# Performance work log

Hardware: AMD Instinct MI355X
Metric: run time of the kernel (lower is better)

Reference implementation:

```python
import jax, jax.numpy as jnp
import numpy as np

B, S, D, H = 2, 2048, 1024, 16
DK = D // H  # 64


def setup_inputs() -> dict:
    key = jax.random.key(0)
    ks = jax.random.split(key, 8)
    q = jax.random.normal(ks[0], (B, S, D), dtype=jnp.float32)
    k = jax.random.normal(ks[1], (B, S, D), dtype=jnp.float32)
    v = jax.random.normal(ks[2], (B, S, D), dtype=jnp.float32)
    mask = jax.random.randint(ks[3], (B, 1, S, S), 0, 2, dtype=jnp.int32)
    scale = 1.0 / np.sqrt(D)
    Wq = jax.random.normal(ks[4], (D, D), dtype=jnp.float32) * scale
    Wk = jax.random.normal(ks[5], (D, D), dtype=jnp.float32) * scale
    Wv = jax.random.normal(ks[6], (D, D), dtype=jnp.float32) * scale
    Wo = jax.random.normal(ks[7], (D, D), dtype=jnp.float32) * scale
    return {"q": q, "k": k, "v": v, "mask": mask,
            "Wq": Wq, "Wk": Wk, "Wv": Wv, "Wo": Wo}


def reference(q, k, v, mask, Wq, Wk, Wv, Wo):
    # Linear projections (torch nn.Linear: x @ W.T, no bias)
    qh = (q @ Wq.T).reshape(B, S, H, DK).transpose(0, 2, 1, 3)  # [B,H,S,DK]
    kh = (k @ Wk.T).reshape(B, S, H, DK).transpose(0, 2, 1, 3)
    vh = (v @ Wv.T).reshape(B, S, H, DK).transpose(0, 2, 1, 3)
    # Scaled dot-product attention with mask fill of -1e9 where mask == 0
    scores = jnp.einsum('bhqd,bhkd->bhqk', qh, kh) / jnp.sqrt(jnp.float32(DK))
    scores = jnp.where(mask == 0, jnp.float32(-1e9), scores)
    attn = jax.nn.softmax(scores, axis=-1)
    ctx = jnp.einsum('bhqk,bhkd->bhqd', attn, vh)  # [B,H,S,DK]
    ctx = ctx.transpose(0, 2, 1, 3).reshape(B, S, D)
    return ctx @ Wo.T
```

## Files before the change

### kernel.cpp

```cpp
#include <hip/hip_runtime.h>

using u16    = unsigned short;
using u32    = unsigned int;
using f32x4  = __attribute__((ext_vector_type(4))) float;
using f32x16 = __attribute__((ext_vector_type(16))) float;
using bf16x8 = __attribute__((ext_vector_type(8))) __bf16;
using u16x4  = __attribute__((ext_vector_type(4))) u16;
using u16x8  = __attribute__((ext_vector_type(8))) u16;
using u32x2  = __attribute__((ext_vector_type(2))) u32;
using u32x4  = __attribute__((ext_vector_type(4))) u32;
using i32x4  = __attribute__((ext_vector_type(4))) int;


__device__ __forceinline__ u16 f2bf(float f) {
  union { __bf16 b; u16 u; } c; c.b = (__bf16)f; return c.u;
}

typedef __attribute__((address_space(1))) const void GVoid;
typedef __attribute__((address_space(3))) void LVoid;

__device__ __forceinline__ void gload_lds16(const void* g, void* l) {
  __builtin_amdgcn_global_load_lds((GVoid*)g, (LVoid*)l, 16, 0, 0);
}

__global__ void cvt_w(const float* __restrict__ a, const float* __restrict__ b,
                      const float* __restrict__ c, const float* __restrict__ dd,
                      u16* __restrict__ oa, u16* __restrict__ ob,
                      u16* __restrict__ oc, u16* __restrict__ od) {
  int y = blockIdx.y;
  const float* s = (y == 0) ? a : (y == 1) ? b : (y == 2) ? c : dd;
  u16* d = (y == 0) ? oa : (y == 1) ? ob : (y == 2) ? oc : od;
  int i = blockIdx.x * 256 + threadIdx.x;
  f32x4 v = ((const f32x4*)s)[i];
  u16x4 r;
#pragma unroll
  for (int j = 0; j < 4; ++j) r[j] = f2bf(v[j]);
  ((u16x4*)d)[i] = r;
}

__global__ void pack_mask(const int* __restrict__ m, u32* __restrict__ mp) {
  int tid = blockIdx.x * 256 + threadIdx.x;
  int q = tid & 2047, kt = (tid >> 11) & 31, b = tid >> 16;
  const i32x4* src = (const i32x4*)(m + ((size_t)(b * 2048 + q)) * 2048 + kt * 64);
  u32 w0 = 0, w1 = 0;
#pragma unroll
  for (int j = 0; j < 8; ++j) {
    i32x4 a = src[j], c = src[j + 8];
#pragma unroll
    for (int e = 0; e < 4; ++e) {
      w0 |= (a[e] != 0 ? 1u : 0u) << (j * 4 + e);
      w1 |= (c[e] != 0 ? 1u : 0u) << (j * 4 + e);
    }
  }
  ((u32x2*)mp)[((size_t)(b * 32 + kt)) * 2048 + q] = u32x2{w0, w1};
}

__global__ __launch_bounds__(256, 3) void gemm_qkv(const float* __restrict__ Aq,
                                                   const float* __restrict__ Ak,
                                                   const float* __restrict__ Av,
                                                   const u16* __restrict__ Wb,
                                                   u16* __restrict__ out) {
  __shared__ alignas(16) char lds[49152];
  const int t = threadIdx.x;
  const int lane = t & 63, wid = t >> 6;
  const int g = lane >> 4, r16 = lane & 15;
  const int wm = wid >> 1, wn = wid & 1;
  const int m0 = blockIdx.x * 128, n0 = blockIdx.y * 128;
  const int z = blockIdx.z;

  const float* Axf = (z == 0) ? Aq : (z == 1) ? Ak : Av;
  const char* Ab = (const char*)Axf;
  const char* Bb = (const char*)(Wb + (size_t)z * 1048576);
  u16* op = out + (size_t)z * 4194304;
  const float qsc = (z == 0) ? 0.18033688011f : 1.0f;

  f32x4 acc[4][4] = {};

  for (int kk = 0; kk < 1024; kk += 64) {
#pragma unroll
    for (int i = 0; i < 8; ++i) {
      int ci = i * 256 + t;
      int row = ci >> 4;
      int pc = ci & 15;
      int lc = pc ^ (row & 15);
      gload_lds16(Ab + (size_t)(m0 + row) * 4096 + kk * 4 + lc * 16, lds + ci * 16);
    }
#pragma unroll
    for (int i = 0; i < 4; ++i) {
      int ci = i * 256 + t;
      int row = ci >> 3;
      int cbs = ((ci & 7) << 4) ^ ((row & 7) << 4);
      gload_lds16(Bb + (size_t)(n0 + row) * 2048 + kk * 2 + cbs, lds + 32768 + ci * 16);
    }
    __syncthreads();
#pragma unroll
    for (int kc = 0; kc < 2; ++kc) {
      bf16x8 af[4], bfr[4];
#pragma unroll
      for (int mf = 0; mf < 4; ++mf) {
        int row = wm * 64 + mf * 16 + r16;
        const char* arow = lds + row * 256;
        int x = row & 15;
        int lc0 = 8 * kc + 2 * g;
        f32x4 alo = *(const f32x4*)(arow + ((lc0 ^ x) * 16));
        f32x4 ahi = *(const f32x4*)(arow + (((lc0 + 1) ^ x) * 16));
        u16x8 pk;
#pragma unroll
        for (int j = 0; j < 4; ++j) { pk[j] = f2bf(alo[j]); pk[4 + j] = f2bf(ahi[j]); }
        af[mf] = __builtin_bit_cast(bf16x8, pk);
      }
#pragma unroll
      for (int nf = 0; nf < 4; ++nf) {
        int row = wn * 64 + nf * 16 + r16;
        bfr[nf] = *(const bf16x8*)(lds + 32768 + row * 128 +
                                   ((64 * kc + 16 * g) ^ ((row & 7) << 4)));
      }
#pragma unroll
      for (int mf = 0; mf < 4; ++mf)
#pragma unroll
        for (int nf = 0; nf < 4; ++nf)
          acc[mf][nf] = __builtin_amdgcn_mfma_f32_16x16x32_bf16(af[mf], bfr[nf], acc[mf][nf], 0, 0, 0);
    }
    __syncthreads();
  }

#pragma unroll
  for (int mf = 0; mf < 4; ++mf) {
#pragma unroll
    for (int nf = 0; nf < 4; ++nf) {
      int mb = m0 + wm * 64 + mf * 16 + 4 * g;
      int n = n0 + wn * 64 + nf * 16 + r16;
      if (z == 0) {
        int bb = mb >> 11, h = n >> 6, dk = n & 63;
#pragma unroll
        for (int r = 0; r < 4; ++r) {
          int s2 = (mb + r) & 2047;
          op[((size_t)(bb * 16 + h) * 2048 + s2) * 64 + dk] = f2bf(acc[mf][nf][r] * qsc);
        }
      } else if (z == 1) {
        int h = n >> 6, dk = n & 63;
#pragma unroll
        for (int r = 0; r < 4; ++r) {
          int m = mb + r;
          int bb = m >> 11, s2 = m & 2047;
          size_t off16 = ((((size_t)(bb * 16 + h) * 32 + (s2 >> 6)) * 2 + ((s2 >> 5) & 1)) * 8 +
                          (dk >> 3)) * 32 + (s2 & 31);
          op[off16 * 8 + (dk & 7)] = f2bf(acc[mf][nf][r]);
        }
      } else {
        int bb = mb >> 11, s2 = mb & 2047, h = n >> 6, d = n & 63;
        size_t off16 = ((((size_t)(bb * 16 + h) * 32 + (s2 >> 6)) * 8 + ((s2 & 63) >> 3)) * 2 +
                        (d >> 5)) * 32 + (d & 31);
        u16x4 pv;
#pragma unroll
        for (int r = 0; r < 4; ++r) pv[r] = f2bf(acc[mf][nf][r]);
        *(u16x4*)(op + off16 * 8 + (s2 & 7)) = pv;
      }
    }
  }
}

__global__ __launch_bounds__(256, 2) void gemm_out(const u16* __restrict__ X,
                                                   const u16* __restrict__ W,
                                                   float* __restrict__ out) {
  __shared__ alignas(16) char lds[32768];
  const int t = threadIdx.x;
  const int lane = t & 63, wid = t >> 6;
  const int g = lane >> 4, r16 = lane & 15;
  const int wm = wid >> 1, wn = wid & 1;
  const int m0 = blockIdx.x * 128, n0 = blockIdx.y * 128;
  const char* Ab = (const char*)X;
  const char* Bb = (const char*)W;

  f32x4 acc[4][4] = {};

  for (int kk = 0; kk < 1024; kk += 64) {
#pragma unroll
    for (int i = 0; i < 4; ++i) {
      int ci = i * 256 + t;
      int row = ci >> 3;
      int cbs = ((ci & 7) << 4) ^ ((row & 7) << 4);
      gload_lds16(Ab + (size_t)(m0 + row) * 2048 + kk * 2 + cbs, lds + ci * 16);
      gload_lds16(Bb + (size_t)(n0 + row) * 2048 + kk * 2 + cbs, lds + 16384 + ci * 16);
    }
    __syncthreads();
#pragma unroll
    for (int kc = 0; kc < 2; ++kc) {
      bf16x8 af[4], bfr[4];
#pragma unroll
      for (int mf = 0; mf < 4; ++mf) {
        int row = wm * 64 + mf * 16 + r16;
        af[mf] = *(const bf16x8*)(lds + row * 128 + ((64 * kc + 16 * g) ^ ((row & 7) << 4)));
      }
#pragma unroll
      for (int nf = 0; nf < 4; ++nf) {
        int row = wn * 64 + nf * 16 + r16;
        bfr[nf] = *(const bf16x8*)(lds + 16384 + row * 128 + ((64 * kc + 16 * g) ^ ((row & 7) << 4)));
      }
#pragma unroll
      for (int mf = 0; mf < 4; ++mf)
#pragma unroll
        for (int nf = 0; nf < 4; ++nf)
          acc[mf][nf] = __builtin_amdgcn_mfma_f32_16x16x32_bf16(af[mf], bfr[nf], acc[mf][nf], 0, 0, 0);
    }
    __syncthreads();
  }

#pragma unroll
  for (int mf = 0; mf < 4; ++mf)
#pragma unroll
    for (int nf = 0; nf < 4; ++nf) {
      int mb = m0 + wm * 64 + mf * 16 + 4 * g;
      int n = n0 + wn * 64 + nf * 16 + r16;
#pragma unroll
      for (int r = 0; r < 4; ++r) out[(size_t)(mb + r) * 1024 + n] = acc[mf][nf][r];
    }
}

struct KH { bf16x8 k[4]; };

__device__ __forceinline__ void loadKh(KH& f, const char* p) {
#pragma unroll
  for (int c = 0; c < 4; ++c) f.k[c] = *(const bf16x8*)(p + c * 1024);
}

__device__ __forceinline__ void attn_body(const bf16x8 (&qf)[4], KH& cur, KH& nxt,
                                          const char*& kp, const char*& vp,
                                          const u32x2*& mptr, u32x2& mcur,
                                          int kh, int hi,
                                          f32x16& o0, f32x16& o1, float& l_run) {
  bf16x8 v00 = *(const bf16x8*)(vp);
  bf16x8 v01 = *(const bf16x8*)(vp + 512);
  bf16x8 v10 = *(const bf16x8*)(vp + 2048);
  bf16x8 v11 = *(const bf16x8*)(vp + 2560);
  loadKh(nxt, kp);
  u32x2 mnext = *mptr;
  kp += 8192; vp += 8192; mptr += 2048;
  __builtin_amdgcn_sched_barrier(0);

  f32x16 s = {};
#pragma unroll
  for (int c = 0; c < 4; ++c)
    s = __builtin_amdgcn_mfma_f32_32x32x16_bf16(cur.k[c], qf[c], s, 0, 0, 0);

  u32 wm = (kh ? mcur.y : mcur.x) >> (4 * hi);
  float ps = 0.f;
#pragma unroll
  for (int r = 0; r < 16; ++r) {
    const int bit = (r & 3) + 8 * (r >> 2);
    float p = __builtin_amdgcn_exp2f(s[r]);
    int sm = ((int)(wm << (31 - bit))) >> 31;
    p = __uint_as_float(__float_as_uint(p) & (u32)sm);
    s[r] = p;
    ps += p;
  }
  l_run += ps;

  u32 w[8];
#pragma unroll
  for (int ss = 0; ss < 2; ++ss) {
    u32 A0, B0, A1, B1;
    asm("v_cvt_pk_bf16_f32 %0, %1, %2" : "=v"(A0) : "v"(s[8*ss+0]), "v"(s[8*ss+1]));
    asm("v_cvt_pk_bf16_f32 %0, %1, %2" : "=v"(B0) : "v"(s[8*ss+2]), "v"(s[8*ss+3]));
    asm("v_cvt_pk_bf16_f32 %0, %1, %2" : "=v"(A1) : "v"(s[8*ss+4]), "v"(s[8*ss+5]));
    asm("v_cvt_pk_bf16_f32 %0, %1, %2" : "=v"(B1) : "v"(s[8*ss+6]), "v"(s[8*ss+7]));
    asm("v_permlane32_swap_b32 %0, %1" : "+v"(A0), "+v"(A1));
    asm("v_permlane32_swap_b32 %0, %1" : "+v"(B0), "+v"(B1));
    w[4*ss+0] = A0; w[4*ss+1] = B0; w[4*ss+2] = A1; w[4*ss+3] = B1;
  }

  bf16x8 pa0 = __builtin_bit_cast(bf16x8, u32x4{w[0], w[1], w[2], w[3]});
  bf16x8 pa1 = __builtin_bit_cast(bf16x8, u32x4{w[4], w[5], w[6], w[7]});
  o0 = __builtin_amdgcn_mfma_f32_32x32x16_bf16(pa0, v00, o0, 0, 0, 0);
  o1 = __builtin_amdgcn_mfma_f32_32x32x16_bf16(pa0, v01, o1, 0, 0, 0);
  o0 = __builtin_amdgcn_mfma_f32_32x32x16_bf16(pa1, v10, o0, 0, 0, 0);
  o1 = __builtin_amdgcn_mfma_f32_32x32x16_bf16(pa1, v11, o1, 0, 0, 0);
  mcur = mnext;
}

__global__ __launch_bounds__(256, 3) void attn_kern(const u16* __restrict__ Qh,
                                                    const u16* __restrict__ Kh,
                                                    const u16* __restrict__ Vt,
                                                    const u32* __restrict__ mp,
                                                    u16* __restrict__ ctx) {
  __shared__ float cmb[2][32][64];
  __shared__ float cmbl[2][64];
  const int t = threadIdx.x;
  const int wid = t >> 6, lane = t & 63;
  const int qw = wid & 1, kh = wid >> 1;
  const int hi = lane >> 5, l31 = lane & 31;

  const int wg = (blockIdx.x & 7) * 128 + (blockIdx.x >> 3);
  const int qt = wg & 31, bh = wg >> 5;
  const int b = bh >> 4, h = bh & 15;

  const char* qbytes = (const char*)Qh;
  const int qbase = qt * 64 + qw * 32;
  const int qg = qbase + l31;

  bf16x8 qf[4];
#pragma unroll
  for (int c = 0; c < 4; ++c)
    qf[c] = *(const bf16x8*)(qbytes + ((size_t)bh * 2048 + qg) * 128 + 32 * c + 16 * hi);

  const char* kp = (const char*)Kh + (size_t)bh * 262144 + kh * 4096 + hi * 512 + l31 * 16;
  const char* vp = (const char*)Vt + (size_t)bh * 262144 + (size_t)(4 * kh + hi) * 1024 + l31 * 16;
  const u32x2* mptr = (const u32x2*)mp + (size_t)b * 65536 + qg;

  f32x16 o0 = {}, o1 = {};
  float l_run = 0.f;

  KH A, B2;
  loadKh(A, kp);
  kp += 8192;
  u32x2 mcur = *mptr;
  mptr += 2048;

#pragma unroll 1
  for (int it = 0; it < 16; ++it) {
    attn_body(qf, A, B2, kp, vp, mptr, mcur, kh, hi, o0, o1, l_run);
    attn_body(qf, B2, A, kp, vp, mptr, mcur, kh, hi, o0, o1, l_run);
  }

  l_run += __shfl_xor(l_run, 32, 64);

  if (kh) {
#pragma unroll
    for (int r = 0; r < 16; ++r) {
      cmb[qw][r][lane]      = o0[r];
      cmb[qw][16 + r][lane] = o1[r];
    }
    cmbl[qw][lane] = l_run;
  }
  __syncthreads();
  if (!kh) {
#pragma unroll
    for (int r = 0; r < 16; ++r) {
      o0[r] += cmb[qw][r][lane];
      o1[r] += cmb[qw][16 + r][lane];
    }
    l_run += cmbl[qw][lane];

    float rl = 1.f / l_run;
#pragma unroll
    for (int r = 0; r < 16; ++r) {
      float rv = __shfl(rl, (r & 3) + 8 * (r >> 2) + 4 * hi, 64);
      int q = qbase + (r & 3) + 8 * (r >> 2) + 4 * hi;
      size_t rowp = ((size_t)b * 2048 + q) * 1024 + h * 64 + l31;
      ctx[rowp]      = f2bf(o0[r] * rv);
      ctx[rowp + 32] = f2bf(o1[r] * rv);
    }
  }
}

extern "C" void kernel_launch(void* const* d_in, const int* in_sizes, int n_in,
                              void* d_out, int out_size, void* d_ws, size_t ws_size,
                              hipStream_t stream) {
  const float* q  = (const float*)d_in[0];
  const float* k  = (const float*)d_in[1];
  const float* v  = (const float*)d_in[2];
  const int* mask = (const int*)d_in[3];
  const float* Wq = (const float*)d_in[4];
  const float* Wk = (const float*)d_in[5];
  const float* Wv = (const float*)d_in[6];
  const float* Wo = (const float*)d_in[7];

  u16* ws = (u16*)d_ws;
  const size_t NX = (size_t)4096 * 1024;
  const size_t NW = (size_t)1024 * 1024;
  u16* Wqb = ws + 3 * NX;
  u16* Qh  = Wqb + 4 * NW;
  u16* ctx = Qh + 3 * NX;
  u32* mpk = (u32*)ws;

  cvt_w<<<dim3(1024, 4), 256, 0, stream>>>(Wq, Wk, Wv, Wo,
                                           Wqb, Wqb + NW, Wqb + 2 * NW, Wqb + 3 * NW);
  pack_mask<<<dim3(512), 256, 0, stream>>>(mask, mpk);
  gemm_qkv<<<dim3(32, 8, 3), 256, 0, stream>>>(q, k, v, Wqb, Qh);
  attn_kern<<<dim3(1024), 256, 0, stream>>>(Qh, Qh + NX, Qh + 2 * NX, mpk, ctx);
  gemm_out<<<dim3(32, 8), 256, 0, stream>>>(ctx, Wqb + 3 * NW, (float*)d_out);
}
```

Before: 126.1 us.

## Process two query sub-tiles per wave to reuse K/V fragments

```diff
diff --git a/kernel.cpp b/kernel.cpp
--- a/kernel.cpp
+++ b/kernel.cpp
@@ -224,26 +224,7 @@
   for (int c = 0; c < 4; ++c) f.k[c] = *(const bf16x8*)(p + c * 1024);
 }
 
-__device__ __forceinline__ void attn_body(const bf16x8 (&qf)[4], KH& cur, KH& nxt,
-                                          const char*& kp, const char*& vp,
-                                          const u32x2*& mptr, u32x2& mcur,
-                                          int kh, int hi,
-                                          f32x16& o0, f32x16& o1, float& l_run) {
-  bf16x8 v00 = *(const bf16x8*)(vp);
-  bf16x8 v01 = *(const bf16x8*)(vp + 512);
-  bf16x8 v10 = *(const bf16x8*)(vp + 2048);
-  bf16x8 v11 = *(const bf16x8*)(vp + 2560);
-  loadKh(nxt, kp);
-  u32x2 mnext = *mptr;
-  kp += 8192; vp += 8192; mptr += 2048;
-  __builtin_amdgcn_sched_barrier(0);
-
-  f32x16 s = {};
-#pragma unroll
-  for (int c = 0; c < 4; ++c)
-    s = __builtin_amdgcn_mfma_f32_32x32x16_bf16(cur.k[c], qf[c], s, 0, 0, 0);
-
-  u32 wm = (kh ? mcur.y : mcur.x) >> (4 * hi);
+__device__ __forceinline__ void sm_cvt(f32x16& s, u32 wm, float& lr, u32 (&w)[8]) {
   float ps = 0.f;
 #pragma unroll
   for (int r = 0; r < 16; ++r) {
@@ -254,9 +235,7 @@
     s[r] = p;
     ps += p;
   }
-  l_run += ps;
-
-  u32 w[8];
+  lr += ps;
 #pragma unroll
   for (int ss = 0; ss < 2; ++ss) {
     u32 A0, B0, A1, B1;
@@ -268,87 +247,144 @@
     asm("v_permlane32_swap_b32 %0, %1" : "+v"(B0), "+v"(B1));
     w[4*ss+0] = A0; w[4*ss+1] = B0; w[4*ss+2] = A1; w[4*ss+3] = B1;
   }
-
-  bf16x8 pa0 = __builtin_bit_cast(bf16x8, u32x4{w[0], w[1], w[2], w[3]});
-  bf16x8 pa1 = __builtin_bit_cast(bf16x8, u32x4{w[4], w[5], w[6], w[7]});
-  o0 = __builtin_amdgcn_mfma_f32_32x32x16_bf16(pa0, v00, o0, 0, 0, 0);
-  o1 = __builtin_amdgcn_mfma_f32_32x32x16_bf16(pa0, v01, o1, 0, 0, 0);
-  o0 = __builtin_amdgcn_mfma_f32_32x32x16_bf16(pa1, v10, o0, 0, 0, 0);
-  o1 = __builtin_amdgcn_mfma_f32_32x32x16_bf16(pa1, v11, o1, 0, 0, 0);
-  mcur = mnext;
-}
-
-__global__ __launch_bounds__(256, 3) void attn_kern(const u16* __restrict__ Qh,
+}
+
+__device__ __forceinline__ void attn_body(const bf16x8 (&qfa)[4], const bf16x8 (&qfb)[4],
+                                          KH& cur, KH& nxt,
+                                          const char*& kp, const char*& vp,
+                                          const u32x2*& mpa, const u32x2*& mpb,
+                                          u32x2& mca, u32x2& mcb,
+                                          int kh, int hi,
+                                          f32x16& oa0, f32x16& oa1,
+                                          f32x16& ob0, f32x16& ob1,
+                                          float& lra, float& lrb) {
+  bf16x8 v00 = *(const bf16x8*)(vp);
+  bf16x8 v01 = *(const bf16x8*)(vp + 512);
+  bf16x8 v10 = *(const bf16x8*)(vp + 2048);
+  bf16x8 v11 = *(const bf16x8*)(vp + 2560);
+  loadKh(nxt, kp);
+  u32x2 mna = *mpa;
+  u32x2 mnb = *mpb;
+  kp += 8192; vp += 8192; mpa += 2048; mpb += 2048;
+  __builtin_amdgcn_sched_barrier(0);
+
+  f32x16 sa = {}, sb = {};
+#pragma unroll
+  for (int c = 0; c < 4; ++c) {
+    sa = __builtin_amdgcn_mfma_f32_32x32x16_bf16(cur.k[c], qfa[c], sa, 0, 0, 0);
+    sb = __builtin_amdgcn_mfma_f32_32x32x16_bf16(cur.k[c], qfb[c], sb, 0, 0, 0);
+  }
+
+  u32 wma = (kh ? mca.y : mca.x) >> (4 * hi);
+  u32 wmb = (kh ? mcb.y : mcb.x) >> (4 * hi);
+  u32 wa[8], wb[8];
+  sm_cvt(sa, wma, lra, wa);
+  sm_cvt(sb, wmb, lrb, wb);
+
+  bf16x8 pa0 = __builtin_bit_cast(bf16x8, u32x4{wa[0], wa[1], wa[2], wa[3]});
+  bf16x8 pa1 = __builtin_bit_cast(bf16x8, u32x4{wa[4], wa[5], wa[6], wa[7]});
+  bf16x8 pb0 = __builtin_bit_cast(bf16x8, u32x4{wb[0], wb[1], wb[2], wb[3]});
+  bf16x8 pb1 = __builtin_bit_cast(bf16x8, u32x4{wb[4], wb[5], wb[6], wb[7]});
+  oa0 = __builtin_amdgcn_mfma_f32_32x32x16_bf16(pa0, v00, oa0, 0, 0, 0);
+  ob0 = __builtin_amdgcn_mfma_f32_32x32x16_bf16(pb0, v00, ob0, 0, 0, 0);
+  oa1 = __builtin_amdgcn_mfma_f32_32x32x16_bf16(pa0, v01, oa1, 0, 0, 0);
+  ob1 = __builtin_amdgcn_mfma_f32_32x32x16_bf16(pb0, v01, ob1, 0, 0, 0);
+  oa0 = __builtin_amdgcn_mfma_f32_32x32x16_bf16(pa1, v10, oa0, 0, 0, 0);
+  ob0 = __builtin_amdgcn_mfma_f32_32x32x16_bf16(pb1, v10, ob0, 0, 0, 0);
+  oa1 = __builtin_amdgcn_mfma_f32_32x32x16_bf16(pa1, v11, oa1, 0, 0, 0);
+  ob1 = __builtin_amdgcn_mfma_f32_32x32x16_bf16(pb1, v11, ob1, 0, 0, 0);
+  mca = mna;
+  mcb = mnb;
+}
+
+__global__ __launch_bounds__(256, 2) void attn_kern(const u16* __restrict__ Qh,
                                                     const u16* __restrict__ Kh,
                                                     const u16* __restrict__ Vt,
                                                     const u32* __restrict__ mp,
                                                     u16* __restrict__ ctx) {
-  __shared__ float cmb[2][32][64];
-  __shared__ float cmbl[2][64];
+  __shared__ float cmb[2][2][32][64];
+  __shared__ float cmbl[2][2][64];
   const int t = threadIdx.x;
   const int wid = t >> 6, lane = t & 63;
   const int qw = wid & 1, kh = wid >> 1;
   const int hi = lane >> 5, l31 = lane & 31;
 
-  const int wg = (blockIdx.x & 7) * 128 + (blockIdx.x >> 3);
-  const int qt = wg & 31, bh = wg >> 5;
+  const int wg = (blockIdx.x & 7) * 64 + (blockIdx.x >> 3);
+  const int qt = wg & 15, bh = wg >> 4;
   const int b = bh >> 4, h = bh & 15;
 
   const char* qbytes = (const char*)Qh;
-  const int qbase = qt * 64 + qw * 32;
-  const int qg = qbase + l31;
-
-  bf16x8 qf[4];
-#pragma unroll
-  for (int c = 0; c < 4; ++c)
-    qf[c] = *(const bf16x8*)(qbytes + ((size_t)bh * 2048 + qg) * 128 + 32 * c + 16 * hi);
+  const int qbase_a = qt * 128 + qw * 64;
+  const int qbase_b = qbase_a + 32;
+  const int qga = qbase_a + l31;
+  const int qgb = qbase_b + l31;
+
+  bf16x8 qfa[4], qfb[4];
+#pragma unroll
+  for (int c = 0; c < 4; ++c) {
+    qfa[c] = *(const bf16x8*)(qbytes + ((size_t)bh * 2048 + qga) * 128 + 32 * c + 16 * hi);
+    qfb[c] = *(const bf16x8*)(qbytes + ((size_t)bh * 2048 + qgb) * 128 + 32 * c + 16 * hi);
+  }
 
   const char* kp = (const char*)Kh + (size_t)bh * 262144 + kh * 4096 + hi * 512 + l31 * 16;
   const char* vp = (const char*)Vt + (size_t)bh * 262144 + (size_t)(4 * kh + hi) * 1024 + l31 * 16;
-  const u32x2* mptr = (const u32x2*)mp + (size_t)b * 65536 + qg;
-
-  f32x16 o0 = {}, o1 = {};
-  float l_run = 0.f;
+  const u32x2* mpa = (const u32x2*)mp + (size_t)b * 65536 + qga;
+  const u32x2* mpb = (const u32x2*)mp + (size_t)b * 65536 + qgb;
+
+  f32x16 oa0 = {}, oa1 = {}, ob0 = {}, ob1 = {};
+  float lra = 0.f, lrb = 0.f;
 
   KH A, B2;
   loadKh(A, kp);
   kp += 8192;
-  u32x2 mcur = *mptr;
-  mptr += 2048;
+  u32x2 mca = *mpa;
+  u32x2 mcb = *mpb;
+  mpa += 2048; mpb += 2048;
 
 #pragma unroll 1
   for (int it = 0; it < 16; ++it) {
-    attn_body(qf, A, B2, kp, vp, mptr, mcur, kh, hi, o0, o1, l_run);
-    attn_body(qf, B2, A, kp, vp, mptr, mcur, kh, hi, o0, o1, l_run);
-  }
-
-  l_run += __shfl_xor(l_run, 32, 64);
+    attn_body(qfa, qfb, A, B2, kp, vp, mpa, mpb, mca, mcb, kh, hi, oa0, oa1, ob0, ob1, lra, lrb);
+    attn_body(qfa, qfb, B2, A, kp, vp, mpa, mpb, mca, mcb, kh, hi, oa0, oa1, ob0, ob1, lra, lrb);
+  }
+
+  lra += __shfl_xor(lra, 32, 64);
+  lrb += __shfl_xor(lrb, 32, 64);
 
   if (kh) {
 #pragma unroll
     for (int r = 0; r < 16; ++r) {
-      cmb[qw][r][lane]      = o0[r];
-      cmb[qw][16 + r][lane] = o1[r];
-    }
-    cmbl[qw][lane] = l_run;
+      cmb[qw][0][r][lane]      = oa0[r];
+      cmb[qw][0][16 + r][lane] = oa1[r];
+      cmb[qw][1][r][lane]      = ob0[r];
+      cmb[qw][1][16 + r][lane] = ob1[r];
+    }
+    cmbl[qw][0][lane] = lra;
+    cmbl[qw][1][lane] = lrb;
   }
   __syncthreads();
   if (!kh) {
 #pragma unroll
     for (int r = 0; r < 16; ++r) {
-      o0[r] += cmb[qw][r][lane];
-      o1[r] += cmb[qw][16 + r][lane];
-    }
-    l_run += cmbl[qw][lane];
-
-    float rl = 1.f / l_run;
+      oa0[r] += cmb[qw][0][r][lane];
+      oa1[r] += cmb[qw][0][16 + r][lane];
+      ob0[r] += cmb[qw][1][r][lane];
+      ob1[r] += cmb[qw][1][16 + r][lane];
+    }
+    lra += cmbl[qw][0][lane];
+    lrb += cmbl[qw][1][lane];
+
+    float rla = 1.f / lra, rlb = 1.f / lrb;
 #pragma unroll
     for (int r = 0; r < 16; ++r) {
-      float rv = __shfl(rl, (r & 3) + 8 * (r >> 2) + 4 * hi, 64);
-      int q = qbase + (r & 3) + 8 * (r >> 2) + 4 * hi;
-      size_t rowp = ((size_t)b * 2048 + q) * 1024 + h * 64 + l31;
-      ctx[rowp]      = f2bf(o0[r] * rv);
-      ctx[rowp + 32] = f2bf(o1[r] * rv);
+      int crow = (r & 3) + 8 * (r >> 2) + 4 * hi;
+      float rva = __shfl(rla, crow, 64);
+      float rvb = __shfl(rlb, crow, 64);
+      size_t rowa = ((size_t)b * 2048 + qbase_a + crow) * 1024 + h * 64 + l31;
+      size_t rowb = ((size_t)b * 2048 + qbase_b + crow) * 1024 + h * 64 + l31;
+      ctx[rowa]      = f2bf(oa0[r] * rva);
+      ctx[rowa + 32] = f2bf(oa1[r] * rva);
+      ctx[rowb]      = f2bf(ob0[r] * rvb);
+      ctx[rowb + 32] = f2bf(ob1[r] * rvb);
     }
   }
 }
@@ -377,6 +413,6 @@
                                            Wqb, Wqb + NW, Wqb + 2 * NW, Wqb + 3 * NW);
   pack_mask<<<dim3(512), 256, 0, stream>>>(mask, mpk);
   gemm_qkv<<<dim3(32, 8, 3), 256, 0, stream>>>(q, k, v, Wqb, Qh);
-  attn_kern<<<dim3(1024), 256, 0, stream>>>(Qh, Qh + NX, Qh + 2 * NX, mpk, ctx);
+  attn_kern<<<dim3(512), 256, 0, stream>>>(Qh, Qh + NX, Qh + 2 * NX, mpk, ctx);
   gemm_out<<<dim3(32, 8), 256, 0, stream>>>(ctx, Wqb + 3 * NW, (float*)d_out);
 }
```

Result: faster. 121.8 us, median of 2 (-3.4%).
